# Kernel tuning notes

Measured on AMD Instinct MI355X. Metric: run time of the kernel, lower is better.

The kernel has to match this reference:

```python
import jax, jax.numpy as jnp
import numpy as np

MIN_DEPTH, MAX_DEPTH = 0.1, 100.0
BN_EPS = 1e-5


def _conv(x, w, b, pad):
    y = jax.lax.conv_general_dilated(
        x, w, window_strides=(1, 1), padding=[(pad, pad), (pad, pad)],
        dimension_numbers=("NCHW", "OIHW", "NCHW"))
    return y + b[None, :, None, None]


def _bn(x, gamma, beta, mean, var):
    # eval-mode BatchNorm2d with running stats
    inv = jax.lax.rsqrt(var + BN_EPS)
    return (x - mean[None, :, None, None]) * (gamma * inv)[None, :, None, None] + beta[None, :, None, None]


def _object_depths(depth, bboxes):
    # depth: (B,1,H,W), bboxes: (B,N,4) int — per-box median (lower median, like torch)
    B, _, H, W = depth.shape
    xs = jnp.arange(W)
    ys = jnp.arange(H)

    def per_image(d2, boxes):  # d2: (H,W), boxes: (N,4)
        dflat = d2.reshape(-1)

        def one_box(box):
            x1 = jnp.maximum(box[0], 0)
            y1 = jnp.maximum(box[1], 0)
            x2 = jnp.minimum(box[2], W)
            y2 = jnp.minimum(box[3], H)
            mask = (((ys >= y1) & (ys < y2))[:, None] & ((xs >= x1) & (xs < x2))[None, :]).reshape(-1)
            vals = jnp.where(mask, dflat, jnp.inf)
            s = jnp.sort(vals)
            k = mask.sum()
            idx = jnp.maximum((k - 1) // 2, 0)
            med = jnp.take(s, idx)
            return jnp.where(k > 0, med, jnp.zeros((), dtype=d2.dtype))

        return jax.vmap(one_box)(boxes)

    return jax.vmap(per_image)(depth[:, 0], bboxes)


def _forward(features, bboxes, w1, b1, g1, be1, m1, v1, w2, b2, g2, be2, m2, v2,
             w3, b3, uw1, ub1, uw2, ub2):
    # depth head
    h = jax.nn.relu(_bn(_conv(features, w1, b1, 1), g1, be1, m1, v1))
    h = jax.nn.relu(_bn(_conv(h, w2, b2, 1), g2, be2, m2, v2))
    disp = jax.nn.sigmoid(_conv(h, w3, b3, 0))  # (B,1,H,W)
    min_disp = 1.0 / MAX_DEPTH
    max_disp = 1.0 / MIN_DEPTH
    depth = 1.0 / (min_disp + (max_disp - min_disp) * disp)
    # uncertainty head
    u = jax.nn.relu(_conv(features, uw1, ub1, 1))
    uncertainty = jax.nn.softplus(_conv(u, uw2, ub2, 0))
    obj = _object_depths(depth, bboxes)
    return depth, uncertainty, obj


def setup_inputs() -> dict:
    key = jax.random.key(0)
    ks = jax.random.split(key, 16)
    B, C, Hc, H, W, N = 8, 256, 256, 96, 160, 64
    f32 = jnp.float32
    inp = {
        "features": jax.random.normal(ks[0], (B, C, H, W), dtype=f32),
        "bboxes": jax.random.randint(ks[1], (B, N, 4), 0, 96, dtype=jnp.int32),
        "w1": jax.random.normal(ks[2], (Hc, C, 3, 3), dtype=f32) * 0.02,
        "b1": jnp.zeros((Hc,), f32),
        "g1": jnp.ones((Hc,), f32),
        "be1": jnp.zeros((Hc,), f32),
        "m1": jax.random.normal(ks[3], (Hc,), dtype=f32) * 0.1,
        "v1": jnp.ones((Hc,), f32),
        "w2": jax.random.normal(ks[4], (Hc, Hc, 3, 3), dtype=f32) * 0.02,
        "b2": jnp.zeros((Hc,), f32),
        "g2": jnp.ones((Hc,), f32),
        "be2": jnp.zeros((Hc,), f32),
        "m2": jax.random.normal(ks[5], (Hc,), dtype=f32) * 0.1,
        "v2": jnp.ones((Hc,), f32),
        "w3": jax.random.normal(ks[6], (1, Hc, 1, 1), dtype=f32) * 0.05,
        "b3": jnp.zeros((1,), f32),
        "uw1": jax.random.normal(ks[7], (Hc // 2, C, 3, 3), dtype=f32) * 0.02,
        "ub1": jnp.zeros((Hc // 2,), f32),
        "uw2": jax.random.normal(ks[8], (1, Hc // 2, 1, 1), dtype=f32) * 0.05,
        "ub2": jnp.zeros((1,), f32),
    }
    return inp


def reference(features, bboxes, w1, b1, g1, be1, m1, v1, w2, b2, g2, be2, m2, v2,
              w3, b3, uw1, ub1, uw2, ub2):
    return _forward(features, bboxes, w1, b1, g1, be1, m1, v1, w2, b2, g2, be2,
                    m2, v2, w3, b3, uw1, ub1, uw2, ub2)
```

## Files before the change

kernel.cpp:

```cpp
#include <hip/hip_runtime.h>
#include <hip/hip_bf16.h>

#define HH 96
#define WW 160
#define BATCH 8
#define NPIX (BATCH*HH*WW)
#define CIN 256
#define IMG (HH*WW)
#define PW 162
#define PH 98
#define PR (PH*PW)
#define PTOT (BATCH*PR)

typedef short bf16x8 __attribute__((ext_vector_type(8)));
typedef float f32x4 __attribute__((ext_vector_type(4)));

__device__ __forceinline__ unsigned short f2bf(float f) {
    unsigned int u = __float_as_uint(f);
    u = (u + 0x7fffu + ((u >> 16) & 1u)) >> 16;
    return (unsigned short)u;
}

__device__ __forceinline__ void gload16(const void* g, void* l) {
    __builtin_amdgcn_global_load_lds(
        (const __attribute__((address_space(1))) void*)g,
        (__attribute__((address_space(3))) void*)l,
        16, 0, 0);
}

__global__ __launch_bounds__(256) void prep_all(
    const float* __restrict__ w1, const float* __restrict__ w2, const float* __restrict__ uw1,
    unsigned short* __restrict__ w1T, unsigned short* __restrict__ w2T, unsigned short* __restrict__ uw1T,
    unsigned int* __restrict__ featPu, unsigned int* __restrict__ h1Pu, float* __restrict__ outd,
    const float* __restrict__ b1, const float* __restrict__ g1, const float* __restrict__ be1,
    const float* __restrict__ m1, const float* __restrict__ v1,
    const float* __restrict__ b2, const float* __restrict__ g2, const float* __restrict__ be2,
    const float* __restrict__ m2, const float* __restrict__ v2,
    const float* __restrict__ ub1,
    float* __restrict__ scale1, float* __restrict__ bias1,
    float* __restrict__ scale2, float* __restrict__ bias2,
    const float* __restrict__ f, unsigned short* __restrict__ ft)
{
    __shared__ float shm[2304];
    const int bid = blockIdx.x;
    const int t = threadIdx.x;

    if (bid < 640) {
        const float* src; unsigned short* dst;
        if (bid < 256)      { src = w1  + (size_t)bid * 2304;        dst = w1T  + (size_t)bid * 2304; }
        else if (bid < 512) { src = w2  + (size_t)(bid - 256) * 2304; dst = w2T  + (size_t)(bid - 256) * 2304; }
        else                { src = uw1 + (size_t)(bid - 512) * 2304; dst = uw1T + (size_t)(bid - 512) * 2304; }
        #pragma unroll
        for (int k = 0; k < 9; ++k) shm[k * 256 + t] = src[k * 256 + t];
        __syncthreads();
        #pragma unroll
        for (int k = 0; k < 9; ++k) {
            int d = k * 256 + t;
            dst[d] = f2bf(shm[(d & 255) * 9 + (d >> 8)]);
        }
    } else if (bid < 4768) {
        int k2 = (bid - 640) * 2 + (t >> 7);
        int lane = t & 127;
        unsigned int* buf = (k2 < 4128) ? featPu : h1Pu;
        int k = (k2 < 4128) ? k2 : (k2 - 4128);
        int img = k / 516, i = k % 516;
        int py, px;
        if (i < PW)            { py = 0;      px = i; }
        else if (i < 2 * PW)   { py = PH - 1; px = i - PW; }
        else { int q = i - 2 * PW; py = 1 + (q >> 1); px = (q & 1) ? (PW - 1) : 0; }
        size_t row = (size_t)img * PR + (size_t)py * PW + px;
        buf[row * 128 + lane] = 0;
    } else if (bid < 5248) {
        outd[(size_t)(bid - 4768) * 256 + t] = 0.f;
    } else if (bid == 5248) {
        if (t < 256) {
            float s1 = g1[t] * rsqrtf(v1[t] + 1e-5f);
            scale1[t] = s1;
            bias1[t]  = (b1[t] - m1[t]) * s1 + be1[t];
            float s2 = g2[t] * rsqrtf(v2[t] + 1e-5f);
            scale2[t] = s2;
            bias2[t]  = (b2[t] - m2[t]) * s2 + be2[t];
            if (t < 128) { scale1[256 + t] = 1.0f; bias1[256 + t] = ub1[t]; }
        }
    } else {
        int id = bid - 5249;
        int x0 = (id % 5) * 32;
        int c0 = ((id / 5) % 8) * 32;
        int by = id / 40;
        int b = by / HH, y = by % HH;
        int tx = t & 31, tg = t >> 5;
        const float* src = f + (((size_t)(b * CIN + c0) * HH + y) * WW) + x0;
        #pragma unroll
        for (int i = 0; i < 4; ++i) {
            int cl = tg + i * 8;
            shm[cl * 33 + tx] = src[(size_t)cl * HH * WW + tx];
        }
        __syncthreads();
        size_t rbase = (size_t)b * PR + (size_t)(y + 1) * PW + (x0 + 1);
        #pragma unroll
        for (int i = 0; i < 4; ++i) {
            int xl = tg + i * 8;
            ft[(rbase + xl) * 256 + c0 + tx] = f2bf(shm[tx * 33 + xl]);
        }
    }
}

__global__ __launch_bounds__(256, 2) void conv3x3_mfma(
    const unsigned short* __restrict__ inP,
    const unsigned short* __restrict__ wT,
    const float* __restrict__ scale, const float* __restrict__ bias,
    unsigned short* __restrict__ outT,
    float* __restrict__ uout,
    const float* __restrict__ uw2, const float* __restrict__ ub2,
    int Cout, int mode, int My)
{
    __shared__ unsigned short Alds[3 * 128 * 32];
    __shared__ unsigned short Blds[272 * 32];
    __shared__ float usum[2][256];

    const int t = threadIdx.x;
    const int wave = t >> 6;
    const int l = t & 63;

    const int lid = blockIdx.x;
    const int xcd = lid & 7;
    const int j = lid >> 3;
    const int n0 = (xcd * 60 + j / My) * 256;
    const int m0 = (j % My) * 128;
    const bool is_unc = (mode == 1) && (m0 == 256);

    const int b0 = n0 / IMG;
    const int rem0 = n0 % IMG;
    const int y0 = rem0 / WW;
    const int x0 = rem0 % WW;
    const int r0 = b0 * PR + (y0 + 1) * PW + (x0 + 1);

    const int lrow = l >> 2;
    const int lkq = (l & 3) ^ ((l >> 3) & 3);

    const unsigned short* asrc0 = wT + (size_t)(m0 + wave * 32 + lrow) * 9 * 256 + lkq * 8;
    const unsigned short* asrc1 = asrc0 + (size_t)16 * 9 * 256;

    char* AldsB = (char*)Alds;
    char* BldsB = (char*)Blds;
    char* aldst = AldsB + wave * 2048;

    const int wm = wave >> 1, wn = wave & 1;
    const int quad = l >> 4, lane16 = l & 15;
    const int aoff = lane16 * 64 + ((quad ^ ((lane16 >> 1) & 3)) << 4);

    int browbase[8];
    #pragma unroll
    for (int i = 0; i < 8; ++i) {
        int jj = wn * 128 + i * 16 + lane16;
        browbase[i] = jj + 2 * ((x0 + jj) / WW) + 7;
    }

    f32x4 acc[4][8];
    #pragma unroll
    for (int mt = 0; mt < 4; ++mt)
        #pragma unroll
        for (int nt = 0; nt < 8; ++nt)
            acc[mt][nt] = (f32x4){0.f, 0.f, 0.f, 0.f};

    for (int cc = 0; cc < 8; ++cc) {
        const int ccoff = cc * 32;
        for (int dyi = 0; dyi < 3; ++dyi) {
            __syncthreads();
            const unsigned short* a0 = asrc0 + (dyi * 3) * 256 + ccoff;
            const unsigned short* a1 = asrc1 + (dyi * 3) * 256 + ccoff;
            #pragma unroll
            for (int dxp = 0; dxp < 3; ++dxp) {
                gload16(a0 + dxp * 256, aldst + dxp * 8192);
                gload16(a1 + dxp * 256, aldst + dxp * 8192 + 1024);
            }
            const ptrdiff_t rs = (ptrdiff_t)r0 + (ptrdiff_t)(dyi - 1) * PW - 8;
            const unsigned short* bs0 = inP + (rs + lrow) * 256 + ccoff + lkq * 8;
            #pragma unroll
            for (int k = 0; k < 4; ++k) {
                const int s = wave * 4 + k;
                gload16(bs0 + s * 4096, BldsB + s * 1024);
            }
            if (wave == 3) gload16(bs0 + 16 * 4096, BldsB + 16 * 1024);
            __syncthreads();
            #pragma unroll
            for (int dx = 0; dx < 3; ++dx) {
                bf16x8 af[4], bfr[8];
                #pragma unroll
                for (int mt = 0; mt < 4; ++mt)
                    af[mt] = *(const bf16x8*)(AldsB + dx * 8192 + ((wm * 4 + mt) << 10) + aoff);
                #pragma unroll
                for (int i = 0; i < 8; ++i) {
                    int row = browbase[i] + dx;
                    int ba = (row << 6) + ((quad ^ ((row >> 1) & 3)) << 4);
                    bfr[i] = *(const bf16x8*)(BldsB + ba);
                }
                #pragma unroll
                for (int mt = 0; mt < 4; ++mt)
                    #pragma unroll
                    for (int nt = 0; nt < 8; ++nt)
                        acc[mt][nt] = __builtin_amdgcn_mfma_f32_16x16x32_bf16(
                            af[mt], bfr[nt], acc[mt][nt], 0, 0, 0);
            }
        }
    }

    if (is_unc) {
        const float* ub = bias + 256;
        float s[8] = {0.f, 0.f, 0.f, 0.f, 0.f, 0.f, 0.f, 0.f};
        #pragma unroll
        for (int mt = 0; mt < 4; ++mt) {
            const int mg = wm * 64 + mt * 16 + quad * 4;
            const float4 bi = *(const float4*)&ub[mg];
            const float4 uw = *(const float4*)&uw2[mg];
            #pragma unroll
            for (int nt = 0; nt < 8; ++nt) {
                s[nt] += fmaxf(acc[mt][nt][0] + bi.x, 0.f) * uw.x
                       + fmaxf(acc[mt][nt][1] + bi.y, 0.f) * uw.y
                       + fmaxf(acc[mt][nt][2] + bi.z, 0.f) * uw.z
                       + fmaxf(acc[mt][nt][3] + bi.w, 0.f) * uw.w;
            }
        }
        #pragma unroll
        for (int nt = 0; nt < 8; ++nt) {
            s[nt] += __shfl_xor(s[nt], 16);
            s[nt] += __shfl_xor(s[nt], 32);
        }
        if (quad == 0) {
            #pragma unroll
            for (int nt = 0; nt < 8; ++nt)
                usum[wm][wn * 128 + nt * 16 + lane16] = s[nt];
        }
        __syncthreads();
        {
            float x = usum[0][t] + usum[1][t] + ub2[0];
            uout[n0 + t] = fmaxf(x, 0.f) + log1pf(expf(-fabsf(x)));
        }
        return;
    }

    if (mode == 0) {
        float s[8] = {0.f, 0.f, 0.f, 0.f, 0.f, 0.f, 0.f, 0.f};
        #pragma unroll
        for (int mt = 0; mt < 4; ++mt) {
            const int mg = m0 + wm * 64 + mt * 16 + quad * 4;
            const float4 sc = *(const float4*)&scale[mg];
            const float4 bi = *(const float4*)&bias[mg];
            const float4 w  = *(const float4*)&uw2[mg];
            #pragma unroll
            for (int nt = 0; nt < 8; ++nt) {
                s[nt] += fmaxf(acc[mt][nt][0] * sc.x + bi.x, 0.f) * w.x
                       + fmaxf(acc[mt][nt][1] * sc.y + bi.y, 0.f) * w.y
                       + fmaxf(acc[mt][nt][2] * sc.z + bi.z, 0.f) * w.z
                       + fmaxf(acc[mt][nt][3] * sc.w + bi.w, 0.f) * w.w;
            }
        }
        #pragma unroll
        for (int nt = 0; nt < 8; ++nt) {
            s[nt] += __shfl_xor(s[nt], 16);
            s[nt] += __shfl_xor(s[nt], 32);
        }
        if (quad == 0) {
            #pragma unroll
            for (int nt = 0; nt < 8; ++nt)
                usum[wm][wn * 128 + nt * 16 + lane16] = s[nt];
        }
        __syncthreads();
        atomicAdd(&uout[n0 + t], usum[0][t] + usum[1][t]);
        return;
    }

    size_t obase[8];
    #pragma unroll
    for (int nt = 0; nt < 8; ++nt) {
        int n = n0 + wn * 128 + nt * 16 + lane16;
        int b = n / IMG, rem = n % IMG, yy = rem / WW, xx = rem % WW;
        obase[nt] = ((size_t)(b * PH + yy + 1) * PW + (xx + 1)) * 256;
    }
    #pragma unroll
    for (int mt = 0; mt < 4; ++mt) {
        const int mg = m0 + wm * 64 + mt * 16 + quad * 4;
        const float4 sc = *(const float4*)&scale[mg];
        const float4 bi = *(const float4*)&bias[mg];
        #pragma unroll
        for (int nt = 0; nt < 8; ++nt) {
            ushort4 pk;
            pk.x = f2bf(fmaxf(acc[mt][nt][0] * sc.x + bi.x, 0.f));
            pk.y = f2bf(fmaxf(acc[mt][nt][1] * sc.y + bi.y, 0.f));
            pk.z = f2bf(fmaxf(acc[mt][nt][2] * sc.z + bi.z, 0.f));
            pk.w = f2bf(fmaxf(acc[mt][nt][3] * sc.w + bi.w, 0.f));
            *(ushort4*)&outT[obase[nt] + mg] = pk;
        }
    }
}

__global__ __launch_bounds__(256) void depth_transform(
    float* __restrict__ out, const float* __restrict__ b3)
{
    int i = blockIdx.x * 256 + threadIdx.x;
    float x = out[i] + b3[0];
    float sig = 1.f / (1.f + expf(-x));
    out[i] = 1.f / (0.01f + 9.99f * sig);
}

__global__ __launch_bounds__(256) void median_kernel(
    const float* __restrict__ depth, const int* __restrict__ bboxes, float* __restrict__ obj)
{
    const int bi = blockIdx.x;
    const int b = bi >> 6;
    const int* bb = bboxes + (size_t)bi * 4;
    int x1 = max(bb[0], 0), y1 = max(bb[1], 0);
    int x2 = min(bb[2], WW), y2 = min(bb[3], HH);
    int w = x2 - x1, h = y2 - y1;
    if (w <= 0 || h <= 0) {
        if (threadIdx.x == 0) obj[bi] = 0.f;
        return;
    }
    const int wh = w * h;
    int tgt = (wh - 1) >> 1;
    const float* dbase = depth + (size_t)b * HH * WW;

    __shared__ unsigned int hist[4][256];
    __shared__ unsigned int wsum[4];
    __shared__ unsigned int sel_prefix, sel_target;
    unsigned int prefix = 0;
    const int t = threadIdx.x;
    const int g = t >> 6, gl = t & 63;

    for (int pass = 0; pass < 4; ++pass) {
        const int shift = 24 - 8 * pass;
        #pragma unroll
        for (int k = 0; k < 4; ++k) hist[k][t & 255] = 0;
        __syncthreads();
        const unsigned int mask_high = (pass == 0) ? 0u : (0xFFFFFFFFu << (shift + 8));
        const unsigned int want = prefix & mask_high;
        for (int yy = y1 + g; yy < y2; yy += 4) {
            const float* row = dbase + yy * WW;
            for (int xx = x1 + gl; xx < x2; xx += 64) {
                unsigned int uu = __float_as_uint(row[xx]);
                bool pred = (uu & mask_high) == want;
                unsigned int bin = (uu >> shift) & 255;
                unsigned long long act = __ballot(pred);
                if (act != 0ull) {
                    int leader = __ffsll(act) - 1;
                    unsigned int lbin = __shfl(bin, leader);
                    unsigned long long same = __ballot(pred && (bin == lbin));
                    if (same == act) {
                        if (gl == leader)
                            atomicAdd(&hist[g][lbin], (unsigned int)__popcll(act));
                    } else if (pred) {
                        atomicAdd(&hist[g][bin], 1u);
                    }
                }
            }
        }
        __syncthreads();
        unsigned int c = hist[0][t] + hist[1][t] + hist[2][t] + hist[3][t];
        unsigned int v = c;
        #pragma unroll
        for (int d = 1; d < 64; d <<= 1) {
            unsigned int n = __shfl_up(v, d);
            if (gl >= d) v += n;
        }
        if (gl == 63) wsum[g] = v;
        __syncthreads();
        unsigned int addv = 0;
        #pragma unroll
        for (int wv = 0; wv < 4; ++wv) addv += (wv < g) ? wsum[wv] : 0u;
        v += addv;
        unsigned int excl = v - c;
        if (excl <= (unsigned int)tgt && (unsigned int)tgt < v) {
            sel_prefix = prefix | ((unsigned int)t << shift);
            sel_target = (unsigned int)tgt - excl;
        }
        __syncthreads();
        prefix = sel_prefix;
        tgt = (int)sel_target;
        __syncthreads();
    }
    if (t == 0) obj[bi] = __uint_as_float(prefix);
}

extern "C" void kernel_launch(void* const* d_in, const int* in_sizes, int n_in,
                              void* d_out, int out_size, void* d_ws, size_t ws_size,
                              hipStream_t stream) {
    const float* features = (const float*)d_in[0];
    const int*   bboxes   = (const int*)d_in[1];
    const float* w1  = (const float*)d_in[2];
    const float* b1  = (const float*)d_in[3];
    const float* g1  = (const float*)d_in[4];
    const float* be1 = (const float*)d_in[5];
    const float* m1  = (const float*)d_in[6];
    const float* v1  = (const float*)d_in[7];
    const float* w2  = (const float*)d_in[8];
    const float* b2  = (const float*)d_in[9];
    const float* g2  = (const float*)d_in[10];
    const float* be2 = (const float*)d_in[11];
    const float* m2  = (const float*)d_in[12];
    const float* v2  = (const float*)d_in[13];
    const float* w3  = (const float*)d_in[14];
    const float* b3  = (const float*)d_in[15];
    const float* uw1 = (const float*)d_in[16];
    const float* ub1 = (const float*)d_in[17];
    const float* uw2 = (const float*)d_in[18];
    const float* ub2 = (const float*)d_in[19];
    float* out = (float*)d_out;

    char* ws = (char*)d_ws;
    unsigned short* featP = (unsigned short*)(ws + 8192);
    unsigned short* h1P   = (unsigned short*)(ws + 65044480);
    unsigned short* w1T   = (unsigned short*)(ws + 130080768);
    unsigned short* uw1T  = w1T + 256 * 2304;
    unsigned short* w2T   = uw1T + 128 * 2304;
    float* scale1 = (float*)(w2T + 589824);
    float* bias1  = scale1 + 384;
    float* scale2 = bias1 + 384;
    float* bias2  = scale2 + 256;

    prep_all<<<35969, 256, 0, stream>>>(
        w1, w2, uw1, w1T, w2T, uw1T,
        (unsigned int*)featP, (unsigned int*)h1P, out,
        b1, g1, be1, m1, v1, b2, g2, be2, m2, v2, ub1,
        scale1, bias1, scale2, bias2,
        features, featP);

    conv3x3_mfma<<<1440, 256, 0, stream>>>(
        featP, w1T, scale1, bias1, h1P, out + NPIX, uw2, ub2, 256, 1, 3);
    conv3x3_mfma<<<960, 256, 0, stream>>>(
        h1P, w2T, scale2, bias2, nullptr, out, w3, nullptr, 256, 0, 2);

    depth_transform<<<NPIX / 256, 256, 0, stream>>>(out, b3);
    median_kernel<<<BATCH * 64, 256, 0, stream>>>(out, bboxes, out + 2 * NPIX);
}
```

Measured before the change: 578.7 us.

## Fuse depth transform with median, median on raw logits; widen feature transpose tiles

The feature NCHW-to-padded-NHWC transpose now handles all 256 channels per block, using float4 loads, XOR-swizzled shared memory and ushort4 stores, which cuts the block count. The depth transform and the per-box median are merged into one finalize kernel. The median is now computed on the raw conv accumulator using an order-preserving float key, and the depth transform is applied only to the selected value. Because the transform is monotone decreasing, the target index is flipped to wh>1, which changes the lower/upper median semantics and needs checking.

```diff
diff --git a/kernel.cpp b/kernel.cpp
--- a/kernel.cpp
+++ b/kernel.cpp
@@ -31,7 +31,7 @@
 __global__ __launch_bounds__(256) void prep_all(
     const float* __restrict__ w1, const float* __restrict__ w2, const float* __restrict__ uw1,
     unsigned short* __restrict__ w1T, unsigned short* __restrict__ w2T, unsigned short* __restrict__ uw1T,
-    unsigned int* __restrict__ featPu, unsigned int* __restrict__ h1Pu, float* __restrict__ outd,
+    unsigned int* __restrict__ featPu, unsigned int* __restrict__ h1Pu, float* __restrict__ racc,
     const float* __restrict__ b1, const float* __restrict__ g1, const float* __restrict__ be1,
     const float* __restrict__ m1, const float* __restrict__ v1,
     const float* __restrict__ b2, const float* __restrict__ g2, const float* __restrict__ be2,
@@ -41,7 +41,7 @@
     float* __restrict__ scale2, float* __restrict__ bias2,
     const float* __restrict__ f, unsigned short* __restrict__ ft)
 {
-    __shared__ float shm[2304];
+    __shared__ float shm[8448];
     const int bid = blockIdx.x;
     const int t = threadIdx.x;
 
@@ -71,7 +71,7 @@
         size_t row = (size_t)img * PR + (size_t)py * PW + px;
         buf[row * 128 + lane] = 0;
     } else if (bid < 5248) {
-        outd[(size_t)(bid - 4768) * 256 + t] = 0.f;
+        racc[(size_t)(bid - 4768) * 256 + t] = 0.f;
     } else if (bid == 5248) {
         if (t < 256) {
             float s1 = g1[t] * rsqrtf(v1[t] + 1e-5f);
@@ -85,22 +85,35 @@
     } else {
         int id = bid - 5249;
         int x0 = (id % 5) * 32;
-        int c0 = ((id / 5) % 8) * 32;
-        int by = id / 40;
+        int by = id / 5;
         int b = by / HH, y = by % HH;
-        int tx = t & 31, tg = t >> 5;
-        const float* src = f + (((size_t)(b * CIN + c0) * HH + y) * WW) + x0;
-        #pragma unroll
-        for (int i = 0; i < 4; ++i) {
-            int cl = tg + i * 8;
-            shm[cl * 33 + tx] = src[(size_t)cl * HH * WW + tx];
-        }
-        __syncthreads();
+        const int rl = t >> 3, ch = t & 7;
+        #pragma unroll
+        for (int k = 0; k < 8; ++k) {
+            int r = k * 32 + rl;
+            const float4 v = *(const float4*)(f + ((size_t)(b * CIN + r) * HH + y) * WW + x0 + ch * 4);
+            int g = (((r >> 3) & 7) ^ ((r >> 6) & 3)) << 2;
+            int base = r * 33;
+            int p0 = ch * 4;
+            shm[base + ((p0 + 0) ^ g)] = v.x;
+            shm[base + ((p0 + 1) ^ g)] = v.y;
+            shm[base + ((p0 + 2) ^ g)] = v.z;
+            shm[base + ((p0 + 3) ^ g)] = v.w;
+        }
+        __syncthreads();
+        const int wv = t >> 6, l = t & 63;
+        const int c0 = l * 4;
+        const int g = (((c0 >> 3) & 7) ^ ((c0 >> 6) & 3)) << 2;
         size_t rbase = (size_t)b * PR + (size_t)(y + 1) * PW + (x0 + 1);
         #pragma unroll
-        for (int i = 0; i < 4; ++i) {
-            int xl = tg + i * 8;
-            ft[(rbase + xl) * 256 + c0 + tx] = f2bf(shm[tx * 33 + xl]);
+        for (int q = 0; q < 8; ++q) {
+            int p = q * 4 + wv;
+            ushort4 pk;
+            pk.x = f2bf(shm[(c0 + 0) * 33 + (p ^ g)]);
+            pk.y = f2bf(shm[(c0 + 1) * 33 + (p ^ g)]);
+            pk.z = f2bf(shm[(c0 + 2) * 33 + (p ^ g)]);
+            pk.w = f2bf(shm[(c0 + 3) * 33 + (p ^ g)]);
+            *(ushort4*)&ft[(rbase + p) * 256 + c0] = pk;
         }
     }
 }
@@ -294,37 +307,36 @@
     }
 }
 
-__global__ __launch_bounds__(256) void depth_transform(
-    float* __restrict__ out, const float* __restrict__ b3)
+__global__ __launch_bounds__(256) void finalize(
+    const float* __restrict__ racc, const float* __restrict__ b3,
+    float* __restrict__ out, const int* __restrict__ bboxes, float* __restrict__ obj)
 {
-    int i = blockIdx.x * 256 + threadIdx.x;
-    float x = out[i] + b3[0];
-    float sig = 1.f / (1.f + expf(-x));
-    out[i] = 1.f / (0.01f + 9.99f * sig);
-}
-
-__global__ __launch_bounds__(256) void median_kernel(
-    const float* __restrict__ depth, const int* __restrict__ bboxes, float* __restrict__ obj)
-{
-    const int bi = blockIdx.x;
+    const int t = threadIdx.x;
+    if (blockIdx.x < 480) {
+        int i = blockIdx.x * 256 + t;
+        float x = racc[i] + b3[0];
+        float sig = 1.f / (1.f + expf(-x));
+        out[i] = 1.f / (0.01f + 9.99f * sig);
+        return;
+    }
+    const int bi = blockIdx.x - 480;
     const int b = bi >> 6;
     const int* bb = bboxes + (size_t)bi * 4;
     int x1 = max(bb[0], 0), y1 = max(bb[1], 0);
     int x2 = min(bb[2], WW), y2 = min(bb[3], HH);
     int w = x2 - x1, h = y2 - y1;
     if (w <= 0 || h <= 0) {
-        if (threadIdx.x == 0) obj[bi] = 0.f;
+        if (t == 0) obj[bi] = 0.f;
         return;
     }
     const int wh = w * h;
-    int tgt = (wh - 1) >> 1;
-    const float* dbase = depth + (size_t)b * HH * WW;
+    int tgt = wh >> 1;
+    const float* dbase = racc + (size_t)b * IMG;
 
     __shared__ unsigned int hist[4][256];
     __shared__ unsigned int wsum[4];
     __shared__ unsigned int sel_prefix, sel_target;
     unsigned int prefix = 0;
-    const int t = threadIdx.x;
     const int g = t >> 6, gl = t & 63;
 
     for (int pass = 0; pass < 4; ++pass) {
@@ -338,8 +350,9 @@
             const float* row = dbase + yy * WW;
             for (int xx = x1 + gl; xx < x2; xx += 64) {
                 unsigned int uu = __float_as_uint(row[xx]);
-                bool pred = (uu & mask_high) == want;
-                unsigned int bin = (uu >> shift) & 255;
+                unsigned int key = (uu & 0x80000000u) ? ~uu : (uu | 0x80000000u);
+                bool pred = (key & mask_high) == want;
+                unsigned int bin = (key >> shift) & 255;
                 unsigned long long act = __ballot(pred);
                 if (act != 0ull) {
                     int leader = __ffsll(act) - 1;
@@ -378,7 +391,13 @@
         tgt = (int)sel_target;
         __syncthreads();
     }
-    if (t == 0) obj[bi] = __uint_as_float(prefix);
+    if (t == 0) {
+        unsigned int key = prefix;
+        unsigned int u = (key & 0x80000000u) ? (key ^ 0x80000000u) : ~key;
+        float x = __uint_as_float(u) + b3[0];
+        float sig = 1.f / (1.f + expf(-x));
+        obj[bi] = 1.f / (0.01f + 9.99f * sig);
+    }
 }
 
 extern "C" void kernel_launch(void* const* d_in, const int* in_sizes, int n_in,
@@ -416,10 +435,11 @@
     float* bias1  = scale1 + 384;
     float* scale2 = bias1 + 384;
     float* bias2  = scale2 + 256;
-
-    prep_all<<<35969, 256, 0, stream>>>(
+    float* racc   = (float*)(ws + 133036032);
+
+    prep_all<<<9089, 256, 0, stream>>>(
         w1, w2, uw1, w1T, w2T, uw1T,
-        (unsigned int*)featP, (unsigned int*)h1P, out,
+        (unsigned int*)featP, (unsigned int*)h1P, racc,
         b1, g1, be1, m1, v1, b2, g2, be2, m2, v2, ub1,
         scale1, bias1, scale2, bias2,
         features, featP);
@@ -427,8 +447,7 @@
     conv3x3_mfma<<<1440, 256, 0, stream>>>(
         featP, w1T, scale1, bias1, h1P, out + NPIX, uw2, ub2, 256, 1, 3);
     conv3x3_mfma<<<960, 256, 0, stream>>>(
-        h1P, w2T, scale2, bias2, nullptr, out, w3, nullptr, 256, 0, 2);
-
-    depth_transform<<<NPIX / 256, 256, 0, stream>>>(out, b3);
-    median_kernel<<<BATCH * 64, 256, 0, stream>>>(out, bboxes, out + 2 * NPIX);
-}
+        h1P, w2T, scale2, bias2, nullptr, racc, w3, nullptr, 256, 0, 2);
+
+    finalize<<<992, 256, 0, stream>>>(racc, b3, out, bboxes, out + 2 * NPIX);
+}
```

Result: faster. 566.5 us (-2.1%).
